# Kernel tuning notes

Hardware: AMD Instinct MI355X
Metric: run time of the kernel (lower is better)

## Reference

```python
import jax, jax.numpy as jnp
import numpy as np

ALPHA = 0.2  # LeakyReLU negative slope
NEG = -1e12


def setup_inputs() -> dict:
    key = jax.random.key(0)
    ks = jax.random.split(key, 7)
    B, N, Cin, F, H = 4, 2048, 256, 64, 4
    x = jax.random.normal(ks[0], (B, N, Cin), dtype=jnp.float32)
    adj = jax.random.randint(ks[1], (N, N), 0, 2, dtype=jnp.int32)
    W = jax.random.normal(ks[2], (H, Cin, F), dtype=jnp.float32) * (1.414 / np.sqrt(Cin))
    a1 = jax.random.normal(ks[3], (H, F), dtype=jnp.float32) * 0.1
    a2 = jax.random.normal(ks[4], (H, F), dtype=jnp.float32) * 0.1
    Wl = jax.random.normal(ks[5], (F, H * F), dtype=jnp.float32) * (1.0 / np.sqrt(H * F))
    bl = jax.random.normal(ks[6], (F,), dtype=jnp.float32) * 0.01
    return {"x": x, "adj": adj, "W": W, "a1": a1, "a2": a2, "Wl": Wl, "bl": bl}


def leaky(v):
    return jnp.where(v >= 0, v, ALPHA * v)


def reference(x, adj, W, a1, a2, Wl, bl):
    # Eval mode: dropout is a no-op.
    # h: [B,H,N,F] per-head projected features
    h = jnp.einsum("bnc,hcf->bhnf", x, W)
    # additive attention: e[b,h,i,j] = leaky(h_i . a1 + h_j . a2)
    f1 = jnp.einsum("bhnf,hf->bhn", h, a1)  # source term
    f2 = jnp.einsum("bhnf,hf->bhn", h, a2)  # target term
    e = leaky(f1[:, :, :, None] + f2[:, :, None, :])  # [B,H,N,N]
    e = jnp.where(adj[None, None] > 0, e, NEG)
    # NOTE: original softmaxes over dim=1 of [B,N,N], i.e. the i axis (axis=2 here)
    att = jax.nn.softmax(e, axis=2)
    hp = jnp.einsum("bhij,bhjf->bhif", att, h)  # [B,H,N,F]
    hp = jax.nn.relu(hp)  # concat=True heads
    B, H, N, F = hp.shape
    cat = hp.transpose(0, 2, 1, 3).reshape(B, N, H * F)
    out = leaky(cat @ Wl.T + bl)  # n_heads > 1 -> linear + leakyrelu
    return out
```

## Files before the change

kernel.cpp:

```cpp
#include <hip/hip_runtime.h>
#include <hip/hip_bf16.h>
#include <stdint.h>

typedef __attribute__((ext_vector_type(8))) short short8;
typedef __attribute__((ext_vector_type(4))) float f32x4;
typedef uint32_t u32;
typedef uint16_t u16;
typedef uint8_t u8;

#define LOG2E 1.4426950408889634f


__device__ __forceinline__ u16 f2bf(float f){
  union{float f; u32 u;} x; x.f = f;
  u32 r = x.u + 0x7FFFu + ((x.u >> 16) & 1u);
  return (u16)(r >> 16);
}
__device__ __forceinline__ u32 pkbf(float a, float b){
  __hip_bfloat162 h = __float22bfloat162_rn(float2{a, b});
  union{ __hip_bfloat162 h; u32 u; } cv; cv.h = h;
  return cv.u;
}
__device__ __forceinline__ float bflo(u32 cd){ union{u32 u; float f;} v; v.u = cd << 16; return v.f; }
__device__ __forceinline__ float bfhi(u32 cd){ union{u32 u; float f;} v; v.u = cd & 0xFFFF0000u; return v.f; }

__global__ __launch_bounds__(256) void k_front(const float* __restrict__ x,
      const float* __restrict__ W, const float* __restrict__ a1, const float* __restrict__ a2,
      const int* __restrict__ adj,
      u8* __restrict__ adjb, u16* __restrict__ hT,
      float* __restrict__ Aarr, float* __restrict__ Barr,
      float* __restrict__ Cexp, float* __restrict__ Dexp){
  int bid = blockIdx.x, t = threadIdx.x;

  if (bid >= 512){
    int idx = (bid - 512)*256 + t;
    const int4* ap = (const int4*)(adj + (size_t)idx*8);
    int4 v0 = ap[0], v1 = ap[1];
    u32 byte = (u32)(v0.x > 0)        | ((u32)(v0.y > 0) << 1)
             | ((u32)(v0.z > 0) << 2) | ((u32)(v0.w > 0) << 3)
             | ((u32)(v1.x > 0) << 4) | ((u32)(v1.y > 0) << 5)
             | ((u32)(v1.z > 0) << 6) | ((u32)(v1.w > 0) << 7);
    adjb[idx] = (u8)byte;
    return;
  }
  __shared__ u16 WL[64*264];
  int rt = bid & 127, cb = bid >> 7;
  const float* Wh = W + (size_t)cb*16384;
  #pragma unroll 4
  for (int p = 0; p < 16; p++){
    int idx = p*256 + t;
    float4 wv = ((const float4*)Wh)[idx];
    int off = idx*4; int c = off >> 6, f0 = off & 63;
    WL[(f0+0)*264 + c] = f2bf(wv.x);
    WL[(f0+1)*264 + c] = f2bf(wv.y);
    WL[(f0+2)*264 + c] = f2bf(wv.z);
    WL[(f0+3)*264 + c] = f2bf(wv.w);
  }
  __syncthreads();

  int w = t >> 6, l = t & 63;
  int rA = rt*64 + w*16 + (l & 15);
  int kg = (l >> 4) * 8;
  f32x4 acc[4] = {};
  const float* xrow = x + (size_t)rA * 256;
  #pragma unroll
  for (int ks = 0; ks < 8; ks++){
    int c = ks*32 + kg;
    float4 xa = *(const float4*)(xrow + c);
    float4 xb = *(const float4*)(xrow + c + 4);
    union{u32 w[4]; short8 v;} A;
    A.w[0] = pkbf(xa.x, xa.y); A.w[1] = pkbf(xa.z, xa.w);
    A.w[2] = pkbf(xb.x, xb.y); A.w[3] = pkbf(xb.z, xb.w);
    #pragma unroll
    for (int q = 0; q < 4; q++){
      short8 Bf = *(const short8*)&WL[(q*16 + (l & 15))*264 + c];
      acc[q] = __builtin_amdgcn_mfma_f32_16x16x32_bf16(A.v, Bf, acc[q], 0, 0, 0);
    }
  }
  int rb = rt*64 + w*16 + (l >> 4)*4;
  int b = rb >> 11, n = rb & 2047;
  #pragma unroll
  for (int q = 0; q < 4; q++){
    int f = q*16 + (l & 15);
    u32 p0 = pkbf(acc[q][0], acc[q][1]);
    u32 p1 = pkbf(acc[q][2], acc[q][3]);
    u16* dst = hT + ((size_t)(b*4 + cb)*64 + f)*2048 + n;
    *(uint2*)dst = uint2{p0, p1};
  }
  float a1v[4], a2v[4];
  #pragma unroll
  for (int q = 0; q < 4; q++){
    a1v[q] = a1[cb*64 + q*16 + (l & 15)];
    a2v[q] = a2[cb*64 + q*16 + (l & 15)];
  }
  float s1[4], s2[4];
  #pragma unroll
  for (int r = 0; r < 4; r++){
    s1[r] = acc[0][r]*a1v[0] + acc[1][r]*a1v[1] + acc[2][r]*a1v[2] + acc[3][r]*a1v[3];
    s2[r] = acc[0][r]*a2v[0] + acc[1][r]*a2v[1] + acc[2][r]*a2v[2] + acc[3][r]*a2v[3];
  }
  #pragma unroll
  for (int m = 1; m <= 8; m <<= 1){
    #pragma unroll
    for (int r = 0; r < 4; r++){
      s1[r] += __shfl_xor(s1[r], m);
      s2[r] += __shfl_xor(s2[r], m);
    }
  }
  if ((l & 15) == 0){
    #pragma unroll
    for (int r = 0; r < 4; r++){
      int row = rb + r;
      int bb = row >> 11, nn = row & 2047;
      int o = (bb*4 + cb)*2048 + nn;
      float fa = s1[r] * LOG2E;
      Aarr[o] = __builtin_amdgcn_exp2f(fa);
      Barr[o] = __builtin_amdgcn_exp2f(0.2f*fa);
      float fb = s2[r] * LOG2E;
      Cexp[o] = __builtin_amdgcn_exp2f(fb);
      Dexp[o] = __builtin_amdgcn_exp2f(0.2f*fb);
    }
  }
}

__global__ __launch_bounds__(256) void k_colsum(const u32* __restrict__ adjw,
      const float* __restrict__ Aarr, const float* __restrict__ Barr,
      const float* __restrict__ Cexp, const float* __restrict__ Dexp,
      u32* __restrict__ CD){
  __shared__ float AL[2048], BL[2048];
  __shared__ float part[4][64];
  int jt = blockIdx.x;
  int bh = blockIdx.y;
  int t = threadIdx.x;
  int w = t >> 6, l = t & 63;
  {
    const float4* As = (const float4*)(Aarr + bh*2048);
    const float4* Bs = (const float4*)(Barr + bh*2048);
    ((float4*)AL)[t]       = As[t];
    ((float4*)AL)[t + 256] = As[t + 256];
    ((float4*)BL)[t]       = Bs[t];
    ((float4*)BL)[t + 256] = Bs[t + 256];
  }
  int j = jt*64 + l;
  float Cj = Cexp[bh*2048 + j];
  float Dj = Dexp[bh*2048 + j];
  int wi = jt*2 + (l >> 5);
  int shl = 31 - (l & 31);
  __syncthreads();
  const u32* aw = adjw + wi;
  float acc0 = 0.f, acc1 = 0.f;
  int i0 = w * 512;
  #pragma unroll 2
  for (int i = i0; i < i0 + 512; i += 8){
    float av[8], bv[8];
    *(float4*)(av)   = *(const float4*)&AL[i];
    *(float4*)(av+4) = *(const float4*)&AL[i+4];
    *(float4*)(bv)   = *(const float4*)&BL[i];
    *(float4*)(bv+4) = *(const float4*)&BL[i+4];
    u32 m[8];
    #pragma unroll
    for (int k = 0; k < 8; k++) m[k] = aw[(size_t)(i+k)*64];
    #pragma unroll
    for (int k = 0; k < 8; k++){
      float v = fmaxf(av[k]*Cj, bv[k]*Dj);
      float sel = ((int)(m[k] << shl) < 0) ? v : 0.f;
      if (k & 1) acc1 += sel; else acc0 += sel;
    }
  }
  part[w][l] = acc0 + acc1;
  __syncthreads();
  if (t < 64){
    float D = (part[0][l] + part[1][l]) + (part[2][l] + part[3][l]);
    float inv = 1.0f / D;
    CD[bh*2048 + j] = pkbf(Cj * inv, Dj * inv);
  }
}

__global__ __launch_bounds__(256) void k_pv(const u32* __restrict__ adjw, const u16* __restrict__ hT,
      const float* __restrict__ Aarr, const float* __restrict__ Barr,
      const u32* __restrict__ CD, float* __restrict__ part){
  int it = blockIdx.x;
  int bh = blockIdx.y;
  int jh = blockIdx.z;
  int b = bh >> 2, h = bh & 3;
  int t = threadIdx.x;
  int w = t >> 6, l = t & 63;

  __shared__ u16 hTl[64*136];

  int i0 = it*128 + w*32 + (l & 15);
  float Ai0 = Aarr[bh*2048 + i0],      Bi0 = Barr[bh*2048 + i0];
  float Ai1 = Aarr[bh*2048 + i0 + 16], Bi1 = Barr[bh*2048 + i0 + 16];
  const u32* CDr = CD + bh*2048;
  const u16* hTr = hT + (size_t)bh * 64 * 2048;
  int kg = (l >> 4) * 8;
  f32x4 acc[2][4] = {};

  for (int jj = 0; jj < 1024; jj += 128){
    int jc = jh*1024 + jj;
    __syncthreads();
    {
      int f = t >> 2, seg = (t & 3) * 32;
      const u16* src = hTr + (size_t)f*2048 + jc + seg;
      u16* d = hTl + f*136 + seg;
      *(uint4*)(d)      = *(const uint4*)(src);
      *(uint4*)(d + 8)  = *(const uint4*)(src + 8);
      *(uint4*)(d + 16) = *(const uint4*)(src + 16);
      *(uint4*)(d + 24) = *(const uint4*)(src + 24);
    }
    __syncthreads();
    uint4 mw0 = *(const uint4*)(adjw + (size_t)i0*64 + (jc >> 5));
    uint4 mw1 = *(const uint4*)(adjw + (size_t)(i0+16)*64 + (jc >> 5));
    #pragma unroll
    for (int ks = 0; ks < 4; ks++){
      u32 cd[8];
      *(uint4*)(cd)     = *(const uint4*)(CDr + jc + ks*32 + kg);
      *(uint4*)(cd + 4) = *(const uint4*)(CDr + jc + ks*32 + kg + 4);
      u32 w0 = (&mw0.x)[ks] >> kg;
      u32 w1 = (&mw1.x)[ks] >> kg;
      float wv0[8], wv1[8];
      #pragma unroll
      for (int e = 0; e < 8; e++){
        float ca = bflo(cd[e]), db = bfhi(cd[e]);
        float ev0 = fmaxf(Ai0*ca, Bi0*db);
        float ev1 = fmaxf(Ai1*ca, Bi1*db);
        wv0[e] = ((int)(w0 << (31-e)) < 0) ? ev0 : 0.f;
        wv1[e] = ((int)(w1 << (31-e)) < 0) ? ev1 : 0.f;
      }
      union{u32 w[4]; short8 v;} A0, A1;
      A0.w[0] = pkbf(wv0[0], wv0[1]); A0.w[1] = pkbf(wv0[2], wv0[3]);
      A0.w[2] = pkbf(wv0[4], wv0[5]); A0.w[3] = pkbf(wv0[6], wv0[7]);
      A1.w[0] = pkbf(wv1[0], wv1[1]); A1.w[1] = pkbf(wv1[2], wv1[3]);
      A1.w[2] = pkbf(wv1[4], wv1[5]); A1.w[3] = pkbf(wv1[6], wv1[7]);
      #pragma unroll
      for (int q = 0; q < 4; q++){
        short8 Bf = *(const short8*)&hTl[(q*16 + (l & 15))*136 + ks*32 + kg];
        acc[0][q] = __builtin_amdgcn_mfma_f32_16x16x32_bf16(A0.v, Bf, acc[0][q], 0, 0, 0);
        acc[1][q] = __builtin_amdgcn_mfma_f32_16x16x32_bf16(A1.v, Bf, acc[1][q], 0, 0, 0);
      }
    }
  }
  float* pr = part + ((size_t)(jh*4 + b)*2048)*256;
  #pragma unroll
  for (int r = 0; r < 2; r++){
    int nb = it*128 + w*32 + r*16 + (l >> 4)*4;
    #pragma unroll
    for (int q = 0; q < 4; q++){
      int f = h*64 + q*16 + (l & 15);
      #pragma unroll
      for (int rr = 0; rr < 4; rr++){
        pr[(size_t)(nb + rr)*256 + f] = acc[r][q][rr];
      }
    }
  }
}

__global__ __launch_bounds__(256) void k_out(const float* __restrict__ part,
                       const float* __restrict__ Wl, const float* __restrict__ bl,
                       float* __restrict__ out){
  int rt = blockIdx.x;
  int w = threadIdx.x >> 6, l = threadIdx.x & 63;
  int rA = rt*64 + w*16 + (l & 15);
  int b = rA >> 11, n = rA & 2047;
  const float* p0 = part + ((size_t)b*2048 + n)*256;
  const float* p1 = part + ((size_t)(4 + b)*2048 + n)*256;
  int kg = (l >> 4) * 8;
  f32x4 acc[4] = {};
  #pragma unroll
  for (int ks = 0; ks < 8; ks++){
    int c = ks*32 + kg;
    float4 x0 = *(const float4*)(p0 + c);
    float4 x1 = *(const float4*)(p0 + c + 4);
    float4 y0 = *(const float4*)(p1 + c);
    float4 y1 = *(const float4*)(p1 + c + 4);
    float av[8];
    av[0] = fmaxf(x0.x + y0.x, 0.f); av[1] = fmaxf(x0.y + y0.y, 0.f);
    av[2] = fmaxf(x0.z + y0.z, 0.f); av[3] = fmaxf(x0.w + y0.w, 0.f);
    av[4] = fmaxf(x1.x + y1.x, 0.f); av[5] = fmaxf(x1.y + y1.y, 0.f);
    av[6] = fmaxf(x1.z + y1.z, 0.f); av[7] = fmaxf(x1.w + y1.w, 0.f);
    union{u32 w[4]; short8 v;} A;
    A.w[0] = pkbf(av[0], av[1]); A.w[1] = pkbf(av[2], av[3]);
    A.w[2] = pkbf(av[4], av[5]); A.w[3] = pkbf(av[6], av[7]);
    #pragma unroll
    for (int q = 0; q < 4; q++){
      const float* wr = Wl + (size_t)(q*16 + (l & 15))*256 + c;
      float4 u0 = *(const float4*)(wr);
      float4 u1 = *(const float4*)(wr + 4);
      union{u32 w[4]; short8 v;} Bv;
      Bv.w[0] = pkbf(u0.x, u0.y); Bv.w[1] = pkbf(u0.z, u0.w);
      Bv.w[2] = pkbf(u1.x, u1.y); Bv.w[3] = pkbf(u1.z, u1.w);
      acc[q] = __builtin_amdgcn_mfma_f32_16x16x32_bf16(A.v, Bv.v, acc[q], 0, 0, 0);
    }
  }
  int rb = rt*64 + w*16 + (l >> 4)*4;
  #pragma unroll
  for (int q = 0; q < 4; q++){
    int o = q*16 + (l & 15);
    float bv = bl[o];
    #pragma unroll
    for (int r = 0; r < 4; r++){
      float v = acc[q][r] + bv;
      out[(size_t)(rb + r)*64 + o] = fmaxf(v, 0.2f*v);
    }
  }
}

extern "C" void kernel_launch(void* const* d_in, const int* in_sizes, int n_in,
                              void* d_out, int out_size, void* d_ws, size_t ws_size,
                              hipStream_t stream) {
  const float* x  = (const float*)d_in[0];
  const int* adj  = (const int*)d_in[1];
  const float* W  = (const float*)d_in[2];
  const float* a1 = (const float*)d_in[3];
  const float* a2 = (const float*)d_in[4];
  const float* Wl = (const float*)d_in[5];
  const float* bl = (const float*)d_in[6];
  float* out = (float*)d_out;
  char* ws = (char*)d_ws;

  u32* adjw   = (u32*)(ws + 0x0000000);
  u16* hT     = (u16*)(ws + 0x0080000);
  float* part = (float*)(ws + 0x0480000);
  float* Aarr = (float*)(ws + 0x1480000);
  float* Barr = (float*)(ws + 0x14A0000);
  float* Cexp = (float*)(ws + 0x14C0000);
  float* Dexp = (float*)(ws + 0x14E0000);
  u32* CD     = (u32*)(ws + 0x1500000);

  k_front<<<2560, 256, 0, stream>>>(x, W, a1, a2, adj, (u8*)adjw, hT, Aarr, Barr, Cexp, Dexp);
  k_colsum<<<dim3(32, 16), 256, 0, stream>>>(adjw, Aarr, Barr, Cexp, Dexp, CD);
  k_pv<<<dim3(16, 16, 2), 256, 0, stream>>>(adjw, hT, Aarr, Barr, CD, part);
  k_out<<<128, 256, 0, stream>>>(part, Wl, bl, out);
}
```

Measured before the change: 81.18 us.

## Fuse four GAT kernels into one persistent cooperative kernel with grid syncs

Replaces the four separate launches (front projection and adjacency packing, column sums, PV matmul, output linear) with a single cooperative kernel. Phases are separated by grid-wide syncs and work is distributed over persistent blocks. Adjacency is now packed a whole 32-bit word per thread, Wl is pre-converted to bf16 once, and the output stage uses 16-row tiles staged through LDS. This removes launch gaps between stages, at the cost of grid-sync overhead and an occupancy query on the host each call.

```diff
diff --git a/kernel.cpp b/kernel.cpp
--- a/kernel.cpp
+++ b/kernel.cpp
@@ -1,6 +1,9 @@
 #include <hip/hip_runtime.h>
 #include <hip/hip_bf16.h>
+#include <hip/hip_cooperative_groups.h>
 #include <stdint.h>
+
+namespace cg = cooperative_groups;
 
 typedef __attribute__((ext_vector_type(8))) short short8;
 typedef __attribute__((ext_vector_type(4))) float f32x4;
@@ -24,283 +27,285 @@
 __device__ __forceinline__ float bflo(u32 cd){ union{u32 u; float f;} v; v.u = cd << 16; return v.f; }
 __device__ __forceinline__ float bfhi(u32 cd){ union{u32 u; float f;} v; v.u = cd & 0xFFFF0000u; return v.f; }
 
-__global__ __launch_bounds__(256) void k_front(const float* __restrict__ x,
-      const float* __restrict__ W, const float* __restrict__ a1, const float* __restrict__ a2,
-      const int* __restrict__ adj,
-      u8* __restrict__ adjb, u16* __restrict__ hT,
-      float* __restrict__ Aarr, float* __restrict__ Barr,
-      float* __restrict__ Cexp, float* __restrict__ Dexp){
-  int bid = blockIdx.x, t = threadIdx.x;
-
-  if (bid >= 512){
-    int idx = (bid - 512)*256 + t;
-    const int4* ap = (const int4*)(adj + (size_t)idx*8);
-    int4 v0 = ap[0], v1 = ap[1];
-    u32 byte = (u32)(v0.x > 0)        | ((u32)(v0.y > 0) << 1)
-             | ((u32)(v0.z > 0) << 2) | ((u32)(v0.w > 0) << 3)
-             | ((u32)(v1.x > 0) << 4) | ((u32)(v1.y > 0) << 5)
-             | ((u32)(v1.z > 0) << 6) | ((u32)(v1.w > 0) << 7);
-    adjb[idx] = (u8)byte;
-    return;
-  }
-  __shared__ u16 WL[64*264];
-  int rt = bid & 127, cb = bid >> 7;
-  const float* Wh = W + (size_t)cb*16384;
-  #pragma unroll 4
-  for (int p = 0; p < 16; p++){
-    int idx = p*256 + t;
-    float4 wv = ((const float4*)Wh)[idx];
-    int off = idx*4; int c = off >> 6, f0 = off & 63;
-    WL[(f0+0)*264 + c] = f2bf(wv.x);
-    WL[(f0+1)*264 + c] = f2bf(wv.y);
-    WL[(f0+2)*264 + c] = f2bf(wv.z);
-    WL[(f0+3)*264 + c] = f2bf(wv.w);
-  }
-  __syncthreads();
-
-  int w = t >> 6, l = t & 63;
-  int rA = rt*64 + w*16 + (l & 15);
-  int kg = (l >> 4) * 8;
-  f32x4 acc[4] = {};
-  const float* xrow = x + (size_t)rA * 256;
-  #pragma unroll
-  for (int ks = 0; ks < 8; ks++){
-    int c = ks*32 + kg;
-    float4 xa = *(const float4*)(xrow + c);
-    float4 xb = *(const float4*)(xrow + c + 4);
-    union{u32 w[4]; short8 v;} A;
-    A.w[0] = pkbf(xa.x, xa.y); A.w[1] = pkbf(xa.z, xa.w);
-    A.w[2] = pkbf(xb.x, xb.y); A.w[3] = pkbf(xb.z, xb.w);
+struct KP {
+  const float* x; const int* adj; const float* W; const float* a1; const float* a2;
+  const float* Wl; const float* bl; float* out;
+  u32* adjw; u16* hT; float* part;
+  float* Aarr; float* Barr; float* Cexp; float* Dexp; u32* CD; u16* Wlb;
+};
+
+__global__ __launch_bounds__(256, 2) void k_fused(KP p){
+  cg::grid_group gg = cg::this_grid();
+  const int nbid = gridDim.x;
+  const int t = threadIdx.x;
+  const int w = t >> 6, l = t & 63;
+
+  __shared__ union SH {
+    u16 WL[64*264];
+    struct { float AL[2048]; float BL[2048]; float red[4][64]; } cs;
+    u16 hTl[64*136];
+    u16 AD[16*272];
+  } sh;
+
+  for (int task = blockIdx.x; task < 512; task += nbid){
+    __syncthreads();
+    int rt = task & 127, cb = task >> 7;
+    const float* Wh = p.W + (size_t)cb*16384;
+    #pragma unroll 4
+    for (int pp = 0; pp < 16; pp++){
+      int idx = pp*256 + t;
+      float4 wv = ((const float4*)Wh)[idx];
+      int off = idx*4; int c = off >> 6, f0 = off & 63;
+      sh.WL[(f0+0)*264 + c] = f2bf(wv.x);
+      sh.WL[(f0+1)*264 + c] = f2bf(wv.y);
+      sh.WL[(f0+2)*264 + c] = f2bf(wv.z);
+      sh.WL[(f0+3)*264 + c] = f2bf(wv.w);
+    }
+    __syncthreads();
+
+    int rA = rt*64 + w*16 + (l & 15);
+    int kg = (l >> 4) * 8;
+    f32x4 acc[4] = {};
+    const float* xrow = p.x + (size_t)rA * 256;
+    #pragma unroll
+    for (int ks = 0; ks < 8; ks++){
+      int c = ks*32 + kg;
+      float4 xa = *(const float4*)(xrow + c);
+      float4 xb = *(const float4*)(xrow + c + 4);
+      union{u32 w[4]; short8 v;} A;
+      A.w[0] = pkbf(xa.x, xa.y); A.w[1] = pkbf(xa.z, xa.w);
+      A.w[2] = pkbf(xb.x, xb.y); A.w[3] = pkbf(xb.z, xb.w);
+      #pragma unroll
+      for (int q = 0; q < 4; q++){
+        short8 Bf = *(const short8*)&sh.WL[(q*16 + (l & 15))*264 + c];
+        acc[q] = __builtin_amdgcn_mfma_f32_16x16x32_bf16(A.v, Bf, acc[q], 0, 0, 0);
+      }
+    }
+    int rb = rt*64 + w*16 + (l >> 4)*4;
+    int b = rb >> 11, n = rb & 2047;
     #pragma unroll
     for (int q = 0; q < 4; q++){
-      short8 Bf = *(const short8*)&WL[(q*16 + (l & 15))*264 + c];
-      acc[q] = __builtin_amdgcn_mfma_f32_16x16x32_bf16(A.v, Bf, acc[q], 0, 0, 0);
-    }
-  }
-  int rb = rt*64 + w*16 + (l >> 4)*4;
-  int b = rb >> 11, n = rb & 2047;
-  #pragma unroll
-  for (int q = 0; q < 4; q++){
-    int f = q*16 + (l & 15);
-    u32 p0 = pkbf(acc[q][0], acc[q][1]);
-    u32 p1 = pkbf(acc[q][2], acc[q][3]);
-    u16* dst = hT + ((size_t)(b*4 + cb)*64 + f)*2048 + n;
-    *(uint2*)dst = uint2{p0, p1};
-  }
-  float a1v[4], a2v[4];
-  #pragma unroll
-  for (int q = 0; q < 4; q++){
-    a1v[q] = a1[cb*64 + q*16 + (l & 15)];
-    a2v[q] = a2[cb*64 + q*16 + (l & 15)];
-  }
-  float s1[4], s2[4];
-  #pragma unroll
-  for (int r = 0; r < 4; r++){
-    s1[r] = acc[0][r]*a1v[0] + acc[1][r]*a1v[1] + acc[2][r]*a1v[2] + acc[3][r]*a1v[3];
-    s2[r] = acc[0][r]*a2v[0] + acc[1][r]*a2v[1] + acc[2][r]*a2v[2] + acc[3][r]*a2v[3];
-  }
-  #pragma unroll
-  for (int m = 1; m <= 8; m <<= 1){
+      int f = q*16 + (l & 15);
+      u32 p0 = pkbf(acc[q][0], acc[q][1]);
+      u32 p1 = pkbf(acc[q][2], acc[q][3]);
+      u16* dst = p.hT + ((size_t)(b*4 + cb)*64 + f)*2048 + n;
+      *(uint2*)dst = uint2{p0, p1};
+    }
+    float a1v[4], a2v[4];
+    #pragma unroll
+    for (int q = 0; q < 4; q++){
+      a1v[q] = p.a1[cb*64 + q*16 + (l & 15)];
+      a2v[q] = p.a2[cb*64 + q*16 + (l & 15)];
+    }
+    float s1[4], s2[4];
     #pragma unroll
     for (int r = 0; r < 4; r++){
-      s1[r] += __shfl_xor(s1[r], m);
-      s2[r] += __shfl_xor(s2[r], m);
-    }
-  }
-  if ((l & 15) == 0){
+      s1[r] = acc[0][r]*a1v[0] + acc[1][r]*a1v[1] + acc[2][r]*a1v[2] + acc[3][r]*a1v[3];
+      s2[r] = acc[0][r]*a2v[0] + acc[1][r]*a2v[1] + acc[2][r]*a2v[2] + acc[3][r]*a2v[3];
+    }
+    #pragma unroll
+    for (int m = 1; m <= 8; m <<= 1){
+      #pragma unroll
+      for (int r = 0; r < 4; r++){
+        s1[r] += __shfl_xor(s1[r], m);
+        s2[r] += __shfl_xor(s2[r], m);
+      }
+    }
+    if ((l & 15) == 0){
+      #pragma unroll
+      for (int r = 0; r < 4; r++){
+        int row = rb + r;
+        int bb = row >> 11, nn = row & 2047;
+        int o = (bb*4 + cb)*2048 + nn;
+        float fa = s1[r] * LOG2E;
+        p.Aarr[o] = __builtin_amdgcn_exp2f(fa);
+        p.Barr[o] = __builtin_amdgcn_exp2f(0.2f*fa);
+        float fb = s2[r] * LOG2E;
+        p.Cexp[o] = __builtin_amdgcn_exp2f(fb);
+        p.Dexp[o] = __builtin_amdgcn_exp2f(0.2f*fb);
+      }
+    }
+  }
+  for (int idx = blockIdx.x*256 + t; idx < 131072; idx += nbid*256){
+    const int4* ap = (const int4*)(p.adj + (size_t)idx*32);
+    u32 word = 0;
+    #pragma unroll
+    for (int k = 0; k < 8; k++){
+      int4 v = ap[k];
+      word |= ((u32)(v.x > 0) << (k*4))   | ((u32)(v.y > 0) << (k*4+1))
+            | ((u32)(v.z > 0) << (k*4+2)) | ((u32)(v.w > 0) << (k*4+3));
+    }
+    p.adjw[idx] = word;
+  }
+  for (int i = blockIdx.x*256 + t; i < 16384; i += nbid*256) p.Wlb[i] = f2bf(p.Wl[i]);
+
+  __threadfence();
+  gg.sync();
+
+  for (int task = blockIdx.x; task < 512; task += nbid){
+    __syncthreads();
+    int jt = task & 31, bh = task >> 5;
+    {
+      const float4* As = (const float4*)(p.Aarr + bh*2048);
+      const float4* Bs = (const float4*)(p.Barr + bh*2048);
+      ((float4*)sh.cs.AL)[t]       = As[t];
+      ((float4*)sh.cs.AL)[t + 256] = As[t + 256];
+      ((float4*)sh.cs.BL)[t]       = Bs[t];
+      ((float4*)sh.cs.BL)[t + 256] = Bs[t + 256];
+    }
+    int j = jt*64 + l;
+    float Cj = p.Cexp[bh*2048 + j];
+    float Dj = p.Dexp[bh*2048 + j];
+    int wi = jt*2 + (l >> 5);
+    int shl = 31 - (l & 31);
+    __syncthreads();
+    const u32* aw = p.adjw + wi;
+    float acc0 = 0.f, acc1 = 0.f;
+    int i0 = w * 512;
+    #pragma unroll 2
+    for (int i = i0; i < i0 + 512; i += 8){
+      float av[8], bv[8];
+      *(float4*)(av)   = *(const float4*)&sh.cs.AL[i];
+      *(float4*)(av+4) = *(const float4*)&sh.cs.AL[i+4];
+      *(float4*)(bv)   = *(const float4*)&sh.cs.BL[i];
+      *(float4*)(bv+4) = *(const float4*)&sh.cs.BL[i+4];
+      u32 m[8];
+      #pragma unroll
+      for (int k = 0; k < 8; k++) m[k] = aw[(size_t)(i+k)*64];
+      #pragma unroll
+      for (int k = 0; k < 8; k++){
+        float v = fmaxf(av[k]*Cj, bv[k]*Dj);
+        float sel = ((int)(m[k] << shl) < 0) ? v : 0.f;
+        if (k & 1) acc1 += sel; else acc0 += sel;
+      }
+    }
+    sh.cs.red[w][l] = acc0 + acc1;
+    __syncthreads();
+    if (t < 64){
+      float D = (sh.cs.red[0][l] + sh.cs.red[1][l]) + (sh.cs.red[2][l] + sh.cs.red[3][l]);
+      float inv = 1.0f / D;
+      p.CD[bh*2048 + j] = pkbf(Cj * inv, Dj * inv);
+    }
+  }
+
+  __threadfence();
+  gg.sync();
+
+  for (int task = blockIdx.x; task < 512; task += nbid){
+    int it = task & 15, bh = (task >> 4) & 15, jh = task >> 8;
+    int b = bh >> 2, h = bh & 3;
+
+    int i0 = it*128 + w*32 + (l & 15);
+    float Ai0 = p.Aarr[bh*2048 + i0],      Bi0 = p.Barr[bh*2048 + i0];
+    float Ai1 = p.Aarr[bh*2048 + i0 + 16], Bi1 = p.Barr[bh*2048 + i0 + 16];
+    const u32* CDr = p.CD + bh*2048;
+    const u16* hTr = p.hT + (size_t)bh * 64 * 2048;
+    int kg = (l >> 4) * 8;
+    f32x4 acc[2][4] = {};
+
+    for (int jj = 0; jj < 1024; jj += 128){
+      int jc = jh*1024 + jj;
+      __syncthreads();
+      {
+        int f = t >> 2, seg = (t & 3) * 32;
+        const u16* src = hTr + (size_t)f*2048 + jc + seg;
+        u16* d = sh.hTl + f*136 + seg;
+        *(uint4*)(d)      = *(const uint4*)(src);
+        *(uint4*)(d + 8)  = *(const uint4*)(src + 8);
+        *(uint4*)(d + 16) = *(const uint4*)(src + 16);
+        *(uint4*)(d + 24) = *(const uint4*)(src + 24);
+      }
+      __syncthreads();
+      uint4 mw0 = *(const uint4*)(p.adjw + (size_t)i0*64 + (jc >> 5));
+      uint4 mw1 = *(const uint4*)(p.adjw + (size_t)(i0+16)*64 + (jc >> 5));
+      #pragma unroll
+      for (int ks = 0; ks < 4; ks++){
+        u32 cd[8];
+        *(uint4*)(cd)     = *(const uint4*)(CDr + jc + ks*32 + kg);
+        *(uint4*)(cd + 4) = *(const uint4*)(CDr + jc + ks*32 + kg + 4);
+        u32 w0 = (&mw0.x)[ks] >> kg;
+        u32 w1 = (&mw1.x)[ks] >> kg;
+        float wv0[8], wv1[8];
+        #pragma unroll
+        for (int e = 0; e < 8; e++){
+          float ca = bflo(cd[e]), db = bfhi(cd[e]);
+          float ev0 = fmaxf(Ai0*ca, Bi0*db);
+          float ev1 = fmaxf(Ai1*ca, Bi1*db);
+          wv0[e] = ((int)(w0 << (31-e)) < 0) ? ev0 : 0.f;
+          wv1[e] = ((int)(w1 << (31-e)) < 0) ? ev1 : 0.f;
+        }
+        union{u32 w[4]; short8 v;} A0, A1;
+        A0.w[0] = pkbf(wv0[0], wv0[1]); A0.w[1] = pkbf(wv0[2], wv0[3]);
+        A0.w[2] = pkbf(wv0[4], wv0[5]); A0.w[3] = pkbf(wv0[6], wv0[7]);
+        A1.w[0] = pkbf(wv1[0], wv1[1]); A1.w[1] = pkbf(wv1[2], wv1[3]);
+        A1.w[2] = pkbf(wv1[4], wv1[5]); A1.w[3] = pkbf(wv1[6], wv1[7]);
+        #pragma unroll
+        for (int q = 0; q < 4; q++){
+          short8 Bf = *(const short8*)&sh.hTl[(q*16 + (l & 15))*136 + ks*32 + kg];
+          acc[0][q] = __builtin_amdgcn_mfma_f32_16x16x32_bf16(A0.v, Bf, acc[0][q], 0, 0, 0);
+          acc[1][q] = __builtin_amdgcn_mfma_f32_16x16x32_bf16(A1.v, Bf, acc[1][q], 0, 0, 0);
+        }
+      }
+    }
+    float* pr = p.part + ((size_t)(jh*4 + b)*2048)*256;
+    #pragma unroll
+    for (int r = 0; r < 2; r++){
+      int nb = it*128 + w*32 + r*16 + (l >> 4)*4;
+      #pragma unroll
+      for (int q = 0; q < 4; q++){
+        int f = h*64 + q*16 + (l & 15);
+        #pragma unroll
+        for (int rr = 0; rr < 4; rr++){
+          pr[(size_t)(nb + rr)*256 + f] = acc[r][q][rr];
+        }
+      }
+    }
+  }
+
+  __threadfence();
+  gg.sync();
+
+  for (int task = blockIdx.x; task < 512; task += nbid){
+    __syncthreads();
+    int r0 = task*16;
+    {
+      int row = t >> 4, cs0 = (t & 15)*16;
+      int gr = r0 + row; int b = gr >> 11, n = gr & 2047;
+      const float* p0 = p.part + ((size_t)(b*2048) + n)*256 + cs0;
+      const float* p1 = p.part + ((size_t)((4+b)*2048) + n)*256 + cs0;
+      float av[16];
+      #pragma unroll
+      for (int k = 0; k < 4; k++){
+        float4 u0 = *(const float4*)(p0 + k*4);
+        float4 u1 = *(const float4*)(p1 + k*4);
+        av[k*4+0] = fmaxf(u0.x + u1.x, 0.f);
+        av[k*4+1] = fmaxf(u0.y + u1.y, 0.f);
+        av[k*4+2] = fmaxf(u0.z + u1.z, 0.f);
+        av[k*4+3] = fmaxf(u0.w + u1.w, 0.f);
+      }
+      u32 pk[8];
+      #pragma unroll
+      for (int k = 0; k < 8; k++) pk[k] = pkbf(av[2*k], av[2*k+1]);
+      u16* d = &sh.AD[row*272 + cs0];
+      *(uint4*)(d)     = *(uint4*)(pk);
+      *(uint4*)(d + 8) = *(uint4*)(pk + 4);
+    }
+    __syncthreads();
+    int kg = (l >> 4) * 8;
+    f32x4 acc = {};
+    #pragma unroll
+    for (int ks = 0; ks < 8; ks++){
+      int c = ks*32 + kg;
+      short8 Af = *(const short8*)&sh.AD[(l & 15)*272 + c];
+      short8 Bf = *(const short8*)(p.Wlb + (size_t)(w*16 + (l & 15))*256 + c);
+      acc = __builtin_amdgcn_mfma_f32_16x16x32_bf16(Af, Bf, acc, 0, 0, 0);
+    }
+    float bv = p.bl[w*16 + (l & 15)];
     #pragma unroll
     for (int r = 0; r < 4; r++){
-      int row = rb + r;
-      int bb = row >> 11, nn = row & 2047;
-      int o = (bb*4 + cb)*2048 + nn;
-      float fa = s1[r] * LOG2E;
-      Aarr[o] = __builtin_amdgcn_exp2f(fa);
-      Barr[o] = __builtin_amdgcn_exp2f(0.2f*fa);
-      float fb = s2[r] * LOG2E;
-      Cexp[o] = __builtin_amdgcn_exp2f(fb);
-      Dexp[o] = __builtin_amdgcn_exp2f(0.2f*fb);
-    }
-  }
-}
-
-__global__ __launch_bounds__(256) void k_colsum(const u32* __restrict__ adjw,
-      const float* __restrict__ Aarr, const float* __restrict__ Barr,
-      const float* __restrict__ Cexp, const float* __restrict__ Dexp,
-      u32* __restrict__ CD){
-  __shared__ float AL[2048], BL[2048];
-  __shared__ float part[4][64];
-  int jt = blockIdx.x;
-  int bh = blockIdx.y;
-  int t = threadIdx.x;
-  int w = t >> 6, l = t & 63;
-  {
-    const float4* As = (const float4*)(Aarr + bh*2048);
-    const float4* Bs = (const float4*)(Barr + bh*2048);
-    ((float4*)AL)[t]       = As[t];
-    ((float4*)AL)[t + 256] = As[t + 256];
-    ((float4*)BL)[t]       = Bs[t];
-    ((float4*)BL)[t + 256] = Bs[t + 256];
-  }
-  int j = jt*64 + l;
-  float Cj = Cexp[bh*2048 + j];
-  float Dj = Dexp[bh*2048 + j];
-  int wi = jt*2 + (l >> 5);
-  int shl = 31 - (l & 31);
-  __syncthreads();
-  const u32* aw = adjw + wi;
-  float acc0 = 0.f, acc1 = 0.f;
-  int i0 = w * 512;
-  #pragma unroll 2
-  for (int i = i0; i < i0 + 512; i += 8){
-    float av[8], bv[8];
-    *(float4*)(av)   = *(const float4*)&AL[i];
-    *(float4*)(av+4) = *(const float4*)&AL[i+4];
-    *(float4*)(bv)   = *(const float4*)&BL[i];
-    *(float4*)(bv+4) = *(const float4*)&BL[i+4];
-    u32 m[8];
-    #pragma unroll
-    for (int k = 0; k < 8; k++) m[k] = aw[(size_t)(i+k)*64];
-    #pragma unroll
-    for (int k = 0; k < 8; k++){
-      float v = fmaxf(av[k]*Cj, bv[k]*Dj);
-      float sel = ((int)(m[k] << shl) < 0) ? v : 0.f;
-      if (k & 1) acc1 += sel; else acc0 += sel;
-    }
-  }
-  part[w][l] = acc0 + acc1;
-  __syncthreads();
-  if (t < 64){
-    float D = (part[0][l] + part[1][l]) + (part[2][l] + part[3][l]);
-    float inv = 1.0f / D;
-    CD[bh*2048 + j] = pkbf(Cj * inv, Dj * inv);
-  }
-}
-
-__global__ __launch_bounds__(256) void k_pv(const u32* __restrict__ adjw, const u16* __restrict__ hT,
-      const float* __restrict__ Aarr, const float* __restrict__ Barr,
-      const u32* __restrict__ CD, float* __restrict__ part){
-  int it = blockIdx.x;
-  int bh = blockIdx.y;
-  int jh = blockIdx.z;
-  int b = bh >> 2, h = bh & 3;
-  int t = threadIdx.x;
-  int w = t >> 6, l = t & 63;
-
-  __shared__ u16 hTl[64*136];
-
-  int i0 = it*128 + w*32 + (l & 15);
-  float Ai0 = Aarr[bh*2048 + i0],      Bi0 = Barr[bh*2048 + i0];
-  float Ai1 = Aarr[bh*2048 + i0 + 16], Bi1 = Barr[bh*2048 + i0 + 16];
-  const u32* CDr = CD + bh*2048;
-  const u16* hTr = hT + (size_t)bh * 64 * 2048;
-  int kg = (l >> 4) * 8;
-  f32x4 acc[2][4] = {};
-
-  for (int jj = 0; jj < 1024; jj += 128){
-    int jc = jh*1024 + jj;
-    __syncthreads();
-    {
-      int f = t >> 2, seg = (t & 3) * 32;
-      const u16* src = hTr + (size_t)f*2048 + jc + seg;
-      u16* d = hTl + f*136 + seg;
-      *(uint4*)(d)      = *(const uint4*)(src);
-      *(uint4*)(d + 8)  = *(const uint4*)(src + 8);
-      *(uint4*)(d + 16) = *(const uint4*)(src + 16);
-      *(uint4*)(d + 24) = *(const uint4*)(src + 24);
-    }
-    __syncthreads();
-    uint4 mw0 = *(const uint4*)(adjw + (size_t)i0*64 + (jc >> 5));
-    uint4 mw1 = *(const uint4*)(adjw + (size_t)(i0+16)*64 + (jc >> 5));
-    #pragma unroll
-    for (int ks = 0; ks < 4; ks++){
-      u32 cd[8];
-      *(uint4*)(cd)     = *(const uint4*)(CDr + jc + ks*32 + kg);
-      *(uint4*)(cd + 4) = *(const uint4*)(CDr + jc + ks*32 + kg + 4);
-      u32 w0 = (&mw0.x)[ks] >> kg;
-      u32 w1 = (&mw1.x)[ks] >> kg;
-      float wv0[8], wv1[8];
-      #pragma unroll
-      for (int e = 0; e < 8; e++){
-        float ca = bflo(cd[e]), db = bfhi(cd[e]);
-        float ev0 = fmaxf(Ai0*ca, Bi0*db);
-        float ev1 = fmaxf(Ai1*ca, Bi1*db);
-        wv0[e] = ((int)(w0 << (31-e)) < 0) ? ev0 : 0.f;
-        wv1[e] = ((int)(w1 << (31-e)) < 0) ? ev1 : 0.f;
-      }
-      union{u32 w[4]; short8 v;} A0, A1;
-      A0.w[0] = pkbf(wv0[0], wv0[1]); A0.w[1] = pkbf(wv0[2], wv0[3]);
-      A0.w[2] = pkbf(wv0[4], wv0[5]); A0.w[3] = pkbf(wv0[6], wv0[7]);
-      A1.w[0] = pkbf(wv1[0], wv1[1]); A1.w[1] = pkbf(wv1[2], wv1[3]);
-      A1.w[2] = pkbf(wv1[4], wv1[5]); A1.w[3] = pkbf(wv1[6], wv1[7]);
-      #pragma unroll
-      for (int q = 0; q < 4; q++){
-        short8 Bf = *(const short8*)&hTl[(q*16 + (l & 15))*136 + ks*32 + kg];
-        acc[0][q] = __builtin_amdgcn_mfma_f32_16x16x32_bf16(A0.v, Bf, acc[0][q], 0, 0, 0);
-        acc[1][q] = __builtin_amdgcn_mfma_f32_16x16x32_bf16(A1.v, Bf, acc[1][q], 0, 0, 0);
-      }
-    }
-  }
-  float* pr = part + ((size_t)(jh*4 + b)*2048)*256;
-  #pragma unroll
-  for (int r = 0; r < 2; r++){
-    int nb = it*128 + w*32 + r*16 + (l >> 4)*4;
-    #pragma unroll
-    for (int q = 0; q < 4; q++){
-      int f = h*64 + q*16 + (l & 15);
-      #pragma unroll
-      for (int rr = 0; rr < 4; rr++){
-        pr[(size_t)(nb + rr)*256 + f] = acc[r][q][rr];
-      }
-    }
-  }
-}
-
-__global__ __launch_bounds__(256) void k_out(const float* __restrict__ part,
-                       const float* __restrict__ Wl, const float* __restrict__ bl,
-                       float* __restrict__ out){
-  int rt = blockIdx.x;
-  int w = threadIdx.x >> 6, l = threadIdx.x & 63;
-  int rA = rt*64 + w*16 + (l & 15);
-  int b = rA >> 11, n = rA & 2047;
-  const float* p0 = part + ((size_t)b*2048 + n)*256;
-  const float* p1 = part + ((size_t)(4 + b)*2048 + n)*256;
-  int kg = (l >> 4) * 8;
-  f32x4 acc[4] = {};
-  #pragma unroll
-  for (int ks = 0; ks < 8; ks++){
-    int c = ks*32 + kg;
-    float4 x0 = *(const float4*)(p0 + c);
-    float4 x1 = *(const float4*)(p0 + c + 4);
-    float4 y0 = *(const float4*)(p1 + c);
-    float4 y1 = *(const float4*)(p1 + c + 4);
-    float av[8];
-    av[0] = fmaxf(x0.x + y0.x, 0.f); av[1] = fmaxf(x0.y + y0.y, 0.f);
-    av[2] = fmaxf(x0.z + y0.z, 0.f); av[3] = fmaxf(x0.w + y0.w, 0.f);
-    av[4] = fmaxf(x1.x + y1.x, 0.f); av[5] = fmaxf(x1.y + y1.y, 0.f);
-    av[6] = fmaxf(x1.z + y1.z, 0.f); av[7] = fmaxf(x1.w + y1.w, 0.f);
-    union{u32 w[4]; short8 v;} A;
-    A.w[0] = pkbf(av[0], av[1]); A.w[1] = pkbf(av[2], av[3]);
-    A.w[2] = pkbf(av[4], av[5]); A.w[3] = pkbf(av[6], av[7]);
-    #pragma unroll
-    for (int q = 0; q < 4; q++){
-      const float* wr = Wl + (size_t)(q*16 + (l & 15))*256 + c;
-      float4 u0 = *(const float4*)(wr);
-      float4 u1 = *(const float4*)(wr + 4);
-      union{u32 w[4]; short8 v;} Bv;
-      Bv.w[0] = pkbf(u0.x, u0.y); Bv.w[1] = pkbf(u0.z, u0.w);
-      Bv.w[2] = pkbf(u1.x, u1.y); Bv.w[3] = pkbf(u1.z, u1.w);
-      acc[q] = __builtin_amdgcn_mfma_f32_16x16x32_bf16(A.v, Bv.v, acc[q], 0, 0, 0);
-    }
-  }
-  int rb = rt*64 + w*16 + (l >> 4)*4;
-  #pragma unroll
-  for (int q = 0; q < 4; q++){
-    int o = q*16 + (l & 15);
-    float bv = bl[o];
-    #pragma unroll
-    for (int r = 0; r < 4; r++){
-      float v = acc[q][r] + bv;
-      out[(size_t)(rb + r)*64 + o] = fmaxf(v, 0.2f*v);
+      float v = acc[r] + bv;
+      int gr = r0 + (l >> 4)*4 + r;
+      p.out[(size_t)gr*64 + w*16 + (l & 15)] = fmaxf(v, 0.2f*v);
     }
   }
 }
@@ -308,27 +313,32 @@
 extern "C" void kernel_launch(void* const* d_in, const int* in_sizes, int n_in,
                               void* d_out, int out_size, void* d_ws, size_t ws_size,
                               hipStream_t stream) {
-  const float* x  = (const float*)d_in[0];
-  const int* adj  = (const int*)d_in[1];
-  const float* W  = (const float*)d_in[2];
-  const float* a1 = (const float*)d_in[3];
-  const float* a2 = (const float*)d_in[4];
-  const float* Wl = (const float*)d_in[5];
-  const float* bl = (const float*)d_in[6];
-  float* out = (float*)d_out;
   char* ws = (char*)d_ws;
-
-  u32* adjw   = (u32*)(ws + 0x0000000);
-  u16* hT     = (u16*)(ws + 0x0080000);
-  float* part = (float*)(ws + 0x0480000);
-  float* Aarr = (float*)(ws + 0x1480000);
-  float* Barr = (float*)(ws + 0x14A0000);
-  float* Cexp = (float*)(ws + 0x14C0000);
-  float* Dexp = (float*)(ws + 0x14E0000);
-  u32* CD     = (u32*)(ws + 0x1500000);
-
-  k_front<<<2560, 256, 0, stream>>>(x, W, a1, a2, adj, (u8*)adjw, hT, Aarr, Barr, Cexp, Dexp);
-  k_colsum<<<dim3(32, 16), 256, 0, stream>>>(adjw, Aarr, Barr, Cexp, Dexp, CD);
-  k_pv<<<dim3(16, 16, 2), 256, 0, stream>>>(adjw, hT, Aarr, Barr, CD, part);
-  k_out<<<128, 256, 0, stream>>>(part, Wl, bl, out);
+  KP kp;
+  kp.x    = (const float*)d_in[0];
+  kp.adj  = (const int*)d_in[1];
+  kp.W    = (const float*)d_in[2];
+  kp.a1   = (const float*)d_in[3];
+  kp.a2   = (const float*)d_in[4];
+  kp.Wl   = (const float*)d_in[5];
+  kp.bl   = (const float*)d_in[6];
+  kp.out  = (float*)d_out;
+  kp.adjw = (u32*)(ws + 0x0000000);
+  kp.hT   = (u16*)(ws + 0x0080000);
+  kp.part = (float*)(ws + 0x0480000);
+  kp.Aarr = (float*)(ws + 0x1480000);
+  kp.Barr = (float*)(ws + 0x14A0000);
+  kp.Cexp = (float*)(ws + 0x14C0000);
+  kp.Dexp = (float*)(ws + 0x14E0000);
+  kp.CD   = (u32*)(ws + 0x1500000);
+  kp.Wlb  = (u16*)(ws + 0x1520000);
+
+  int maxb = 0;
+  if (hipOccupancyMaxActiveBlocksPerMultiprocessor(&maxb, k_fused, 256, 0) != hipSuccess || maxb < 1)
+    maxb = 1;
+  int grid = maxb * 256;
+  if (grid > 512) grid = 512;
+
+  void* args[] = { &kp };
+  hipLaunchCooperativeKernel((void*)k_fused, dim3(grid), dim3(256), args, 0, stream);
 }
```

After: 275.6 us. 239% more time.

## Swizzle W tile in LDS and widen colsum blocks to 128 columns

Applied to the files above, without the earlier changes.

The projection kernel now XOR-swizzles the column index when staging the bf16 W tile in LDS, and applies the same swizzle on the MFMA B-fragment reads, to reduce bank conflicts. The column-sum kernel now covers 128 columns per block: each thread handles two columns and loads adjacency bitmasks as uint4 instead of single words. This halves the colsum grid and reuses the staged A/B arrays across twice as many columns. The cost is fewer blocks in flight and some extra per-thread select and convert work.

```diff
diff --git a/kernel.cpp b/kernel.cpp
--- a/kernel.cpp
+++ b/kernel.cpp
@@ -51,16 +51,23 @@
     int idx = p*256 + t;
     float4 wv = ((const float4*)Wh)[idx];
     int off = idx*4; int c = off >> 6, f0 = off & 63;
-    WL[(f0+0)*264 + c] = f2bf(wv.x);
-    WL[(f0+1)*264 + c] = f2bf(wv.y);
-    WL[(f0+2)*264 + c] = f2bf(wv.z);
-    WL[(f0+3)*264 + c] = f2bf(wv.w);
+    int cc = c ^ (((f0 >> 2) & 7) << 3);
+    WL[(f0+0)*264 + cc] = f2bf(wv.x);
+    WL[(f0+1)*264 + cc] = f2bf(wv.y);
+    WL[(f0+2)*264 + cc] = f2bf(wv.z);
+    WL[(f0+3)*264 + cc] = f2bf(wv.w);
   }
   __syncthreads();
 
   int w = t >> 6, l = t & 63;
   int rA = rt*64 + w*16 + (l & 15);
   int kg = (l >> 4) * 8;
+  int rowq[4], rswq[4];
+  #pragma unroll
+  for (int q = 0; q < 4; q++){
+    rowq[q] = q*16 + (l & 15);
+    rswq[q] = ((rowq[q] >> 2) & 7) << 3;
+  }
   f32x4 acc[4] = {};
   const float* xrow = x + (size_t)rA * 256;
   #pragma unroll
@@ -73,7 +80,7 @@
     A.w[2] = pkbf(xb.x, xb.y); A.w[3] = pkbf(xb.z, xb.w);
     #pragma unroll
     for (int q = 0; q < 4; q++){
-      short8 Bf = *(const short8*)&WL[(q*16 + (l & 15))*264 + c];
+      short8 Bf = *(const short8*)&WL[rowq[q]*264 + (c ^ rswq[q])];
       acc[q] = __builtin_amdgcn_mfma_f32_16x16x32_bf16(A.v, Bf, acc[q], 0, 0, 0);
     }
   }
@@ -128,7 +135,7 @@
       const float* __restrict__ Cexp, const float* __restrict__ Dexp,
       u32* __restrict__ CD){
   __shared__ float AL[2048], BL[2048];
-  __shared__ float part[4][64];
+  __shared__ float red[4][128];
   int jt = blockIdx.x;
   int bh = blockIdx.y;
   int t = threadIdx.x;
@@ -141,36 +148,45 @@
     ((float4*)BL)[t]       = Bs[t];
     ((float4*)BL)[t + 256] = Bs[t + 256];
   }
-  int j = jt*64 + l;
-  float Cj = Cexp[bh*2048 + j];
-  float Dj = Dexp[bh*2048 + j];
-  int wi = jt*2 + (l >> 5);
-  int shl = 31 - (l & 31);
+  int ja = jt*128 + l;
+  int jb = ja + 64;
+  float Cja = Cexp[bh*2048 + ja], Dja = Dexp[bh*2048 + ja];
+  float Cjb = Cexp[bh*2048 + jb], Djb = Dexp[bh*2048 + jb];
+  bool hiw = (l & 32) != 0;
+  int shr = l & 31;
   __syncthreads();
-  const u32* aw = adjw + wi;
-  float acc0 = 0.f, acc1 = 0.f;
+  const uint4* aw4 = (const uint4*)adjw + jt;
+  float aa0 = 0.f, aa1 = 0.f, ab0 = 0.f, ab1 = 0.f;
   int i0 = w * 512;
   #pragma unroll 2
-  for (int i = i0; i < i0 + 512; i += 8){
-    float av[8], bv[8];
-    *(float4*)(av)   = *(const float4*)&AL[i];
-    *(float4*)(av+4) = *(const float4*)&AL[i+4];
-    *(float4*)(bv)   = *(const float4*)&BL[i];
-    *(float4*)(bv+4) = *(const float4*)&BL[i+4];
-    u32 m[8];
-    #pragma unroll
-    for (int k = 0; k < 8; k++) m[k] = aw[(size_t)(i+k)*64];
-    #pragma unroll
-    for (int k = 0; k < 8; k++){
-      float v = fmaxf(av[k]*Cj, bv[k]*Dj);
-      float sel = ((int)(m[k] << shl) < 0) ? v : 0.f;
-      if (k & 1) acc1 += sel; else acc0 += sel;
-    }
-  }
-  part[w][l] = acc0 + acc1;
+  for (int i = i0; i < i0 + 512; i += 4){
+    uint4 m0 = aw4[(size_t)(i+0)*16];
+    uint4 m1 = aw4[(size_t)(i+1)*16];
+    uint4 m2 = aw4[(size_t)(i+2)*16];
+    uint4 m3 = aw4[(size_t)(i+3)*16];
+    float av[4], bv[4];
+    *(float4*)(av) = *(const float4*)&AL[i];
+    *(float4*)(bv) = *(const float4*)&BL[i];
+    uint4 mm[4] = {m0, m1, m2, m3};
+    #pragma unroll
+    for (int k = 0; k < 4; k++){
+      u32 wa = hiw ? mm[k].y : mm[k].x;
+      u32 wb = hiw ? mm[k].w : mm[k].z;
+      float va = fmaxf(av[k]*Cja, bv[k]*Dja);
+      float vb = fmaxf(av[k]*Cjb, bv[k]*Djb);
+      float ba = (float)((wa >> shr) & 1u);
+      float bb2 = (float)((wb >> shr) & 1u);
+      if (k & 1){ aa1 = fmaf(va, ba, aa1); ab1 = fmaf(vb, bb2, ab1); }
+      else      { aa0 = fmaf(va, ba, aa0); ab0 = fmaf(vb, bb2, ab0); }
+    }
+  }
+  red[w][l]      = aa0 + aa1;
+  red[w][64 + l] = ab0 + ab1;
   __syncthreads();
-  if (t < 64){
-    float D = (part[0][l] + part[1][l]) + (part[2][l] + part[3][l]);
+  if (t < 128){
+    float D = (red[0][t] + red[1][t]) + (red[2][t] + red[3][t]);
+    int j = jt*128 + t;
+    float Cj = Cexp[bh*2048 + j], Dj = Dexp[bh*2048 + j];
     float inv = 1.0f / D;
     CD[bh*2048 + j] = pkbf(Cj * inv, Dj * inv);
   }
@@ -328,7 +344,7 @@
   u32* CD     = (u32*)(ws + 0x1500000);
 
   k_front<<<2560, 256, 0, stream>>>(x, W, a1, a2, adj, (u8*)adjw, hT, Aarr, Barr, Cexp, Dexp);
-  k_colsum<<<dim3(32, 16), 256, 0, stream>>>(adjw, Aarr, Barr, Cexp, Dexp, CD);
+  k_colsum<<<dim3(16, 16), 256, 0, stream>>>(adjw, Aarr, Barr, Cexp, Dexp, CD);
   k_pv<<<dim3(16, 16, 2), 256, 0, stream>>>(adjw, hT, Aarr, Barr, CD, part);
   k_out<<<128, 256, 0, stream>>>(part, Wl, bl, out);
 }
```

Result: slower. 149.4 us (+84.0%).
